# Kernel tuning notes

Measured on AMD Instinct MI355X. Metric: run time of the kernel, lower is better.

Reference implementation:

```python
import jax, jax.numpy as jnp
import numpy as np

SIZE = 1024      # codebook size
DIM = 64         # latent_dim
TOPK = 3
BETA_C = 0.25
LEGACY = False

def setup_inputs() -> dict:
    key = jax.random.key(0)
    kz, ke = jax.random.split(key)
    z = jax.random.normal(kz, (16, 64, 64, DIM), dtype=jnp.float32)
    # nn.Embedding init: uniform(-1/size, 1/size)
    emb = jax.random.uniform(ke, (SIZE, DIM), minval=-1.0 / SIZE, maxval=1.0 / SIZE, dtype=jnp.float32)
    return {"z": z, "emb": emb}

def reference(z, emb):
    zf = z.reshape(-1, DIM)                                  # [N, D]
    # squared euclidean distances via matmul expansion: [N, SIZE]
    d = (jnp.sum(zf ** 2, axis=1, keepdims=True)
         + jnp.sum(emb ** 2, axis=1)
         - 2.0 * (zf @ emb.T))
    neg_d, topk_idx = jax.lax.top_k(-d, TOPK)                # smallest distances -> [N, K]
    # direct gather instead of one-hot matmul (same math)
    z_q = jnp.mean(emb[topk_idx], axis=1).reshape(z.shape)   # [N,K,D] -> [N,D] -> z.shape
    if LEGACY:
        loss = (jnp.mean((jax.lax.stop_gradient(z_q) - z) ** 2)
                + BETA_C * jnp.mean((z_q - jax.lax.stop_gradient(z)) ** 2))
    else:
        loss = (BETA_C * jnp.mean((jax.lax.stop_gradient(z_q) - z) ** 2)
                + jnp.mean((z_q - jax.lax.stop_gradient(z)) ** 2))
    # one-hot encodings are part of the module's return signature
    topk_encodings = jax.nn.one_hot(topk_idx, SIZE, dtype=z.dtype)   # [N, K, SIZE]
    e_mean = jnp.mean(topk_encodings, axis=(0, 1))                   # [SIZE]
    perplexity = jnp.exp(-jnp.sum(e_mean * jnp.log(e_mean + 1e-10)))
    z_q_st = z + jax.lax.stop_gradient(z_q - z)              # straight-through estimator
    return (z_q_st, loss, perplexity, topk_encodings, topk_idx)
```

## Files before the change

kernel.cpp:

```cpp
#include <hip/hip_runtime.h>
#include <math.h>

#define N_ROWS 65536
#define CB 1024
#define SPLITS 4
#define JS (CB / SPLITS)

__device__ __forceinline__ float tree_sum64_sq(const float* x) {
#pragma clang fp contract(off)
    float sq[64];
#pragma unroll
    for (int i = 0; i < 64; ++i) sq[i] = x[i] * x[i];
    float s[16];
#pragma unroll
    for (int l = 0; l < 16; ++l) s[l] = (sq[l] + sq[l + 16]) + (sq[l + 32] + sq[l + 48]);
    float t[8];
#pragma unroll
    for (int l = 0; l < 8; ++l) t[l] = s[l] + s[l + 8];
    float u[4];
#pragma unroll
    for (int l = 0; l < 4; ++l) u[l] = t[l] + t[l + 4];
    float v0 = u[0] + u[2];
    float v1 = u[1] + u[3];
    return v0 + v1;
}

__device__ __forceinline__ void top3_insert(float d, int j,
                                            float& v0, float& v1, float& v2,
                                            int& i0, int& i1, int& i2) {
    bool b0 = d < v0, b1 = d < v1, b2 = d < v2;
    v2 = b1 ? v1 : (b2 ? d : v2);
    i2 = b1 ? i1 : (b2 ? j : i2);
    v1 = b0 ? v0 : (b1 ? d : v1);
    i1 = b0 ? i0 : (b1 ? j : i1);
    v0 = b0 ? d : v0;
    i0 = b0 ? j : i0;
}

__global__ __launch_bounds__(256) void embB_kernel(const float* __restrict__ emb,
                                                   float* __restrict__ B) {
    int j = blockIdx.x * 256 + threadIdx.x;
    if (j >= CB) return;
    float e[64];
    const float4* e4 = (const float4*)(emb + (size_t)j * 64);
#pragma unroll
    for (int k = 0; k < 16; ++k) {
        float4 v = e4[k];
        e[4 * k] = v.x; e[4 * k + 1] = v.y; e[4 * k + 2] = v.z; e[4 * k + 3] = v.w;
    }
    B[j] = tree_sum64_sq(e);
}

__global__ __launch_bounds__(256) void score_kernel(const float* __restrict__ z,
                                                    const float* __restrict__ emb,
                                                    const float* __restrict__ B,
                                                    float* __restrict__ scrD,
                                                    int* __restrict__ scrI) {
    int bid = blockIdx.x;
    int split = bid & (SPLITS - 1);
    int rowBlk = bid >> 2;
    int row = rowBlk * 256 + threadIdx.x;

    float zr[64];
    const float4* z4 = (const float4*)(z + (size_t)row * 64);
#pragma unroll
    for (int k = 0; k < 16; ++k) {
        float4 v = z4[k];
        zr[4 * k] = v.x; zr[4 * k + 1] = v.y; zr[4 * k + 2] = v.z; zr[4 * k + 3] = v.w;
    }
    float A = tree_sum64_sq(zr);

    float v0 = 3.402823466e38f, v1 = 3.402823466e38f, v2 = 3.402823466e38f;
    int i0 = 0, i1 = 0, i2 = 0;
    int jbase = split * JS;

    for (int jj = 0; jj < JS; ++jj) {
        int j = jbase + jj;
        const float4* e4 = (const float4*)(emb + (size_t)j * 64);
        float Bj = B[j];
        float acc = 0.0f;
#pragma unroll
        for (int k = 0; k < 16; ++k) {
            float4 e = e4[k];
            acc = fmaf(zr[4 * k],     e.x, acc);
            acc = fmaf(zr[4 * k + 1], e.y, acc);
            acc = fmaf(zr[4 * k + 2], e.z, acc);
            acc = fmaf(zr[4 * k + 3], e.w, acc);
        }
        float d = (A + Bj) - 2.0f * acc;
        top3_insert(d, j, v0, v1, v2, i0, i1, i2);
    }
    size_t o = ((size_t)split * N_ROWS + row) * 3;
    scrD[o] = v0; scrD[o + 1] = v1; scrD[o + 2] = v2;
    scrI[o] = i0; scrI[o + 1] = i1; scrI[o + 2] = i2;
}

__global__ __launch_bounds__(256) void merge_kernel(const float* __restrict__ z,
                                                    const float* __restrict__ emb,
                                                    const float* __restrict__ scrD,
                                                    const int* __restrict__ scrI,
                                                    float* __restrict__ out0,
                                                    float* __restrict__ out4,
                                                    int* __restrict__ hist,
                                                    float* __restrict__ lossAcc) {
    int row = blockIdx.x * 256 + threadIdx.x;

    float v0 = 3.402823466e38f, v1 = 3.402823466e38f, v2 = 3.402823466e38f;
    int i0 = 0, i1 = 0, i2 = 0;
#pragma unroll
    for (int s = 0; s < SPLITS; ++s) {
        size_t o = ((size_t)s * N_ROWS + row) * 3;
#pragma unroll
        for (int t = 0; t < 3; ++t) {
            float d = scrD[o + t];
            int j = scrI[o + t];
            top3_insert(d, j, v0, v1, v2, i0, i1, i2);
        }
    }

    const float* e0 = emb + (size_t)i0 * 64;
    const float* e1 = emb + (size_t)i1 * 64;
    const float* e2 = emb + (size_t)i2 * 64;
    const float4* z4 = (const float4*)(z + (size_t)row * 64);
    float4* o4 = (float4*)(out0 + (size_t)row * 64);

    float lsum = 0.0f;
#pragma unroll
    for (int k4 = 0; k4 < 16; ++k4) {
        float4 zv = z4[k4];
        float4 st;
        {
            int k = 4 * k4;
            float zq = ((e0[k] + e1[k]) + e2[k]) / 3.0f;
            float df = zq - zv.x;
            st.x = zv.x + df;
            lsum = fmaf(df, df, lsum);
        }
        {
            int k = 4 * k4 + 1;
            float zq = ((e0[k] + e1[k]) + e2[k]) / 3.0f;
            float df = zq - zv.y;
            st.y = zv.y + df;
            lsum = fmaf(df, df, lsum);
        }
        {
            int k = 4 * k4 + 2;
            float zq = ((e0[k] + e1[k]) + e2[k]) / 3.0f;
            float df = zq - zv.z;
            st.z = zv.z + df;
            lsum = fmaf(df, df, lsum);
        }
        {
            int k = 4 * k4 + 3;
            float zq = ((e0[k] + e1[k]) + e2[k]) / 3.0f;
            float df = zq - zv.w;
            st.w = zv.w + df;
            lsum = fmaf(df, df, lsum);
        }
        o4[k4] = st;
    }

    size_t ob = (size_t)row * 3;
    out4[ob]     = (float)i0;
    out4[ob + 1] = (float)i1;
    out4[ob + 2] = (float)i2;
    atomicAdd(&hist[i0], 1);
    atomicAdd(&hist[i1], 1);
    atomicAdd(&hist[i2], 1);

#pragma unroll
    for (int off = 32; off >= 1; off >>= 1) lsum += __shfl_down(lsum, off);
    if ((threadIdx.x & 63) == 0) atomicAdd(lossAcc, lsum);
}

__global__ __launch_bounds__(256) void onehot_kernel(const float* __restrict__ idxf,
                                                     float4* __restrict__ out3) {
    size_t q = (size_t)blockIdx.x * 256 + threadIdx.x;
    int slice = (int)(q >> 8);
    int c0 = (int)(q & 255) * 4;
    int idx = (int)idxf[slice];
    float4 v;
    v.x = (c0     == idx) ? 1.0f : 0.0f;
    v.y = (c0 + 1 == idx) ? 1.0f : 0.0f;
    v.z = (c0 + 2 == idx) ? 1.0f : 0.0f;
    v.w = (c0 + 3 == idx) ? 1.0f : 0.0f;
    out3[q] = v;
}

__global__ __launch_bounds__(256) void finalize_kernel(const int* __restrict__ hist,
                                                       const float* __restrict__ lossAcc,
                                                       float* __restrict__ out1,
                                                       float* __restrict__ out2) {
    __shared__ float red[256];
    int t = threadIdx.x;
    float local = 0.0f;
    for (int b = t; b < CB; b += 256) {
        float em = (float)hist[b] / 196608.0f;
        local += em * logf(em + 1e-10f);
    }
    red[t] = local;
    __syncthreads();
    for (int s = 128; s >= 1; s >>= 1) {
        if (t < s) red[t] += red[t + s];
        __syncthreads();
    }
    if (t == 0) {
        *out2 = expf(-red[0]);
        float m = *lossAcc / 4194304.0f;
        *out1 = 0.25f * m + m;
    }
}

extern "C" void kernel_launch(void* const* d_in, const int* in_sizes, int n_in,
                              void* d_out, int out_size, void* d_ws, size_t ws_size,
                              hipStream_t stream) {
    const float* z   = (const float*)d_in[0];
    const float* emb = (const float*)d_in[1];

    float* out  = (float*)d_out;
    float* out0 = out;
    float* out1 = out + 4194304;
    float* out2 = out + 4194305;
    float* out3 = out + 4194306;
    float* out4 = out + 4194306 + 201326592ll;

    int*   hist    = (int*)d_ws;
    float* lossAcc = (float*)((char*)d_ws + 4096);
    float* B       = (float*)((char*)d_ws + 8192);

    float* scrD = out3;
    int*   scrI = (int*)(out3 + (size_t)SPLITS * N_ROWS * 3);

    hipMemsetAsync(d_ws, 0, 4096 + 16, stream);

    embB_kernel<<<4, 256, 0, stream>>>(emb, B);
    score_kernel<<<(N_ROWS / 256) * SPLITS, 256, 0, stream>>>(z, emb, B, scrD, scrI);
    merge_kernel<<<N_ROWS / 256, 256, 0, stream>>>(z, emb, scrD, scrI, out0, out4,
                                                   hist, lossAcc);
    onehot_kernel<<<196608, 256, 0, stream>>>(out4, (float4*)out3);
    finalize_kernel<<<1, 256, 0, stream>>>(hist, lossAcc, out1, out2);
}
```

Measured before the change: 1.073 ms.

## Fuse score, merge and one-hot kernels into one kernel with interleaved zero-fill

Replaces the split-codebook score kernel, the top-k merge kernel and the one-hot kernel with a single kernel per row block. It scans the full codebook four entries at a time and interleaves zero stores for the block's one-hot region into the distance loop, so the writes overlap the compute. After a barrier it scatters the three ones and reuses the z row held in registers. This drops the scratch round trip, two launches and the separate 800MB one-hot write pass, but cuts grid parallelism fourfold (256 blocks) and relies on the barrier to order zero-fill before the one-hot stores.

```diff
diff --git a/kernel.cpp b/kernel.cpp
--- a/kernel.cpp
+++ b/kernel.cpp
@@ -3,8 +3,6 @@
 
 #define N_ROWS 65536
 #define CB 1024
-#define SPLITS 4
-#define JS (CB / SPLITS)
 
 __device__ __forceinline__ float tree_sum64_sq(const float* x) {
 #pragma clang fp contract(off)
@@ -51,15 +49,16 @@
     B[j] = tree_sum64_sq(e);
 }
 
-__global__ __launch_bounds__(256) void score_kernel(const float* __restrict__ z,
-                                                    const float* __restrict__ emb,
-                                                    const float* __restrict__ B,
-                                                    float* __restrict__ scrD,
-                                                    int* __restrict__ scrI) {
-    int bid = blockIdx.x;
-    int split = bid & (SPLITS - 1);
-    int rowBlk = bid >> 2;
-    int row = rowBlk * 256 + threadIdx.x;
+__global__ __launch_bounds__(256) void mega_kernel(const float* __restrict__ z,
+                                                   const float* __restrict__ emb,
+                                                   const float* __restrict__ B,
+                                                   float* __restrict__ out0,
+                                                   float* __restrict__ out3,
+                                                   float* __restrict__ out4,
+                                                   int* __restrict__ hist,
+                                                   float* __restrict__ lossAcc) {
+    const int t = threadIdx.x;
+    const int row = blockIdx.x * 256 + t;
 
     float zr[64];
     const float4* z4 = (const float4*)(z + (size_t)row * 64);
@@ -70,91 +69,90 @@
     }
     float A = tree_sum64_sq(zr);
 
+    float4* zb = (float4*)out3 + (size_t)blockIdx.x * 196608;
+    const float4 zero4 = make_float4(0.0f, 0.0f, 0.0f, 0.0f);
+
     float v0 = 3.402823466e38f, v1 = 3.402823466e38f, v2 = 3.402823466e38f;
     int i0 = 0, i1 = 0, i2 = 0;
-    int jbase = split * JS;
-
-    for (int jj = 0; jj < JS; ++jj) {
-        int j = jbase + jj;
-        const float4* e4 = (const float4*)(emb + (size_t)j * 64);
-        float Bj = B[j];
-        float acc = 0.0f;
+
+    for (int g = 0; g < 256; ++g) {
+        zb[(size_t)(3 * g + 0) * 256 + t] = zero4;
+        zb[(size_t)(3 * g + 1) * 256 + t] = zero4;
+        zb[(size_t)(3 * g + 2) * 256 + t] = zero4;
+
+        const int j = 4 * g;
+        const float4* e0p = (const float4*)(emb + (size_t)(j + 0) * 64);
+        const float4* e1p = (const float4*)(emb + (size_t)(j + 1) * 64);
+        const float4* e2p = (const float4*)(emb + (size_t)(j + 2) * 64);
+        const float4* e3p = (const float4*)(emb + (size_t)(j + 3) * 64);
+        float b0 = B[j], b1 = B[j + 1], b2 = B[j + 2], b3 = B[j + 3];
+
+        float a0 = 0.0f, a1 = 0.0f, a2 = 0.0f, a3 = 0.0f;
 #pragma unroll
         for (int k = 0; k < 16; ++k) {
-            float4 e = e4[k];
-            acc = fmaf(zr[4 * k],     e.x, acc);
-            acc = fmaf(zr[4 * k + 1], e.y, acc);
-            acc = fmaf(zr[4 * k + 2], e.z, acc);
-            acc = fmaf(zr[4 * k + 3], e.w, acc);
-        }
-        float d = (A + Bj) - 2.0f * acc;
-        top3_insert(d, j, v0, v1, v2, i0, i1, i2);
-    }
-    size_t o = ((size_t)split * N_ROWS + row) * 3;
-    scrD[o] = v0; scrD[o + 1] = v1; scrD[o + 2] = v2;
-    scrI[o] = i0; scrI[o + 1] = i1; scrI[o + 2] = i2;
-}
-
-__global__ __launch_bounds__(256) void merge_kernel(const float* __restrict__ z,
-                                                    const float* __restrict__ emb,
-                                                    const float* __restrict__ scrD,
-                                                    const int* __restrict__ scrI,
-                                                    float* __restrict__ out0,
-                                                    float* __restrict__ out4,
-                                                    int* __restrict__ hist,
-                                                    float* __restrict__ lossAcc) {
-    int row = blockIdx.x * 256 + threadIdx.x;
-
-    float v0 = 3.402823466e38f, v1 = 3.402823466e38f, v2 = 3.402823466e38f;
-    int i0 = 0, i1 = 0, i2 = 0;
-#pragma unroll
-    for (int s = 0; s < SPLITS; ++s) {
-        size_t o = ((size_t)s * N_ROWS + row) * 3;
-#pragma unroll
-        for (int t = 0; t < 3; ++t) {
-            float d = scrD[o + t];
-            int j = scrI[o + t];
-            top3_insert(d, j, v0, v1, v2, i0, i1, i2);
-        }
-    }
+            float4 e0 = e0p[k], e1 = e1p[k], e2 = e2p[k], e3 = e3p[k];
+            float x0 = zr[4 * k], x1 = zr[4 * k + 1], x2 = zr[4 * k + 2], x3 = zr[4 * k + 3];
+            a0 = fmaf(x0, e0.x, a0); a0 = fmaf(x1, e0.y, a0);
+            a0 = fmaf(x2, e0.z, a0); a0 = fmaf(x3, e0.w, a0);
+            a1 = fmaf(x0, e1.x, a1); a1 = fmaf(x1, e1.y, a1);
+            a1 = fmaf(x2, e1.z, a1); a1 = fmaf(x3, e1.w, a1);
+            a2 = fmaf(x0, e2.x, a2); a2 = fmaf(x1, e2.y, a2);
+            a2 = fmaf(x2, e2.z, a2); a2 = fmaf(x3, e2.w, a2);
+            a3 = fmaf(x0, e3.x, a3); a3 = fmaf(x1, e3.y, a3);
+            a3 = fmaf(x2, e3.z, a3); a3 = fmaf(x3, e3.w, a3);
+        }
+        float d0 = (A + b0) - 2.0f * a0;
+        float d1 = (A + b1) - 2.0f * a1;
+        float d2 = (A + b2) - 2.0f * a2;
+        float d3 = (A + b3) - 2.0f * a3;
+        top3_insert(d0, j + 0, v0, v1, v2, i0, i1, i2);
+        top3_insert(d1, j + 1, v0, v1, v2, i0, i1, i2);
+        top3_insert(d2, j + 2, v0, v1, v2, i0, i1, i2);
+        top3_insert(d3, j + 3, v0, v1, v2, i0, i1, i2);
+    }
+
+    __syncthreads();
+
+    size_t rb = (size_t)row * 3072;
+    out3[rb + i0]          = 1.0f;
+    out3[rb + 1024 + i1]   = 1.0f;
+    out3[rb + 2048 + i2]   = 1.0f;
 
     const float* e0 = emb + (size_t)i0 * 64;
     const float* e1 = emb + (size_t)i1 * 64;
     const float* e2 = emb + (size_t)i2 * 64;
-    const float4* z4 = (const float4*)(z + (size_t)row * 64);
     float4* o4 = (float4*)(out0 + (size_t)row * 64);
 
     float lsum = 0.0f;
 #pragma unroll
     for (int k4 = 0; k4 < 16; ++k4) {
-        float4 zv = z4[k4];
         float4 st;
         {
             int k = 4 * k4;
             float zq = ((e0[k] + e1[k]) + e2[k]) / 3.0f;
-            float df = zq - zv.x;
-            st.x = zv.x + df;
+            float df = zq - zr[k];
+            st.x = zr[k] + df;
             lsum = fmaf(df, df, lsum);
         }
         {
             int k = 4 * k4 + 1;
             float zq = ((e0[k] + e1[k]) + e2[k]) / 3.0f;
-            float df = zq - zv.y;
-            st.y = zv.y + df;
+            float df = zq - zr[k];
+            st.y = zr[k] + df;
             lsum = fmaf(df, df, lsum);
         }
         {
             int k = 4 * k4 + 2;
             float zq = ((e0[k] + e1[k]) + e2[k]) / 3.0f;
-            float df = zq - zv.z;
-            st.z = zv.z + df;
+            float df = zq - zr[k];
+            st.z = zr[k] + df;
             lsum = fmaf(df, df, lsum);
         }
         {
             int k = 4 * k4 + 3;
             float zq = ((e0[k] + e1[k]) + e2[k]) / 3.0f;
-            float df = zq - zv.w;
-            st.w = zv.w + df;
+            float df = zq - zr[k];
+            st.w = zr[k] + df;
             lsum = fmaf(df, df, lsum);
         }
         o4[k4] = st;
@@ -170,21 +168,7 @@
 
 #pragma unroll
     for (int off = 32; off >= 1; off >>= 1) lsum += __shfl_down(lsum, off);
-    if ((threadIdx.x & 63) == 0) atomicAdd(lossAcc, lsum);
-}
-
-__global__ __launch_bounds__(256) void onehot_kernel(const float* __restrict__ idxf,
-                                                     float4* __restrict__ out3) {
-    size_t q = (size_t)blockIdx.x * 256 + threadIdx.x;
-    int slice = (int)(q >> 8);
-    int c0 = (int)(q & 255) * 4;
-    int idx = (int)idxf[slice];
-    float4 v;
-    v.x = (c0     == idx) ? 1.0f : 0.0f;
-    v.y = (c0 + 1 == idx) ? 1.0f : 0.0f;
-    v.z = (c0 + 2 == idx) ? 1.0f : 0.0f;
-    v.w = (c0 + 3 == idx) ? 1.0f : 0.0f;
-    out3[q] = v;
+    if ((t & 63) == 0) atomicAdd(lossAcc, lsum);
 }
 
 __global__ __launch_bounds__(256) void finalize_kernel(const int* __restrict__ hist,
@@ -228,15 +212,10 @@
     float* lossAcc = (float*)((char*)d_ws + 4096);
     float* B       = (float*)((char*)d_ws + 8192);
 
-    float* scrD = out3;
-    int*   scrI = (int*)(out3 + (size_t)SPLITS * N_ROWS * 3);
-
     hipMemsetAsync(d_ws, 0, 4096 + 16, stream);
 
     embB_kernel<<<4, 256, 0, stream>>>(emb, B);
-    score_kernel<<<(N_ROWS / 256) * SPLITS, 256, 0, stream>>>(z, emb, B, scrD, scrI);
-    merge_kernel<<<N_ROWS / 256, 256, 0, stream>>>(z, emb, scrD, scrI, out0, out4,
-                                                   hist, lossAcc);
-    onehot_kernel<<<196608, 256, 0, stream>>>(out4, (float4*)out3);
+    mega_kernel<<<N_ROWS / 256, 256, 0, stream>>>(z, emb, B, out0, out3, out4,
+                                                  hist, lossAcc);
     finalize_kernel<<<1, 256, 0, stream>>>(hist, lossAcc, out1, out2);
 }
```

After: 1.712 ms. 1.6x slower.

## Fuse one-hot zero fill into score kernel and scatter ones in merge

Applied to the files above, without the earlier changes.

The separate one-hot kernel that wrote the whole 805MB encodings tensor is removed. The score kernel now interleaves zero-filling its slice of the one-hot output with the distance loop, so those stores overlap with compute, and the merge kernel scatters the three 1.0 entries per row. The scratch top-k buffers move from the output region to the workspace, which avoids a conflict with the zero fill. The inner distance loop is also unrolled over two codebook rows at a time. The change relies on the zero-fill partitioning covering the full tensor and on the workspace being large enough for the scratch buffers.

```diff
diff --git a/kernel.cpp b/kernel.cpp
--- a/kernel.cpp
+++ b/kernel.cpp
@@ -51,15 +51,17 @@
     B[j] = tree_sum64_sq(e);
 }
 
-__global__ __launch_bounds__(256) void score_kernel(const float* __restrict__ z,
-                                                    const float* __restrict__ emb,
-                                                    const float* __restrict__ B,
-                                                    float* __restrict__ scrD,
-                                                    int* __restrict__ scrI) {
-    int bid = blockIdx.x;
-    int split = bid & (SPLITS - 1);
-    int rowBlk = bid >> 2;
-    int row = rowBlk * 256 + threadIdx.x;
+__global__ __launch_bounds__(256) void score_fused_kernel(const float* __restrict__ z,
+                                                          const float* __restrict__ emb,
+                                                          const float* __restrict__ B,
+                                                          float* __restrict__ out3,
+                                                          float* __restrict__ scrD,
+                                                          int* __restrict__ scrI) {
+    const int bid = blockIdx.x;
+    const int split = bid & (SPLITS - 1);
+    const int rowBlk = bid >> 2;
+    const int t = threadIdx.x;
+    const int row = rowBlk * 256 + t;
 
     float zr[64];
     const float4* z4 = (const float4*)(z + (size_t)row * 64);
@@ -70,26 +72,43 @@
     }
     float A = tree_sum64_sq(zr);
 
+    float4* zb = (float4*)out3 + (size_t)rowBlk * 196608 + (size_t)split * 49152;
+    const float4 zero4 = make_float4(0.0f, 0.0f, 0.0f, 0.0f);
+
     float v0 = 3.402823466e38f, v1 = 3.402823466e38f, v2 = 3.402823466e38f;
     int i0 = 0, i1 = 0, i2 = 0;
-    int jbase = split * JS;
-
-    for (int jj = 0; jj < JS; ++jj) {
-        int j = jbase + jj;
-        const float4* e4 = (const float4*)(emb + (size_t)j * 64);
-        float Bj = B[j];
-        float acc = 0.0f;
-#pragma unroll
-        for (int k = 0; k < 16; ++k) {
-            float4 e = e4[k];
-            acc = fmaf(zr[4 * k],     e.x, acc);
-            acc = fmaf(zr[4 * k + 1], e.y, acc);
-            acc = fmaf(zr[4 * k + 2], e.z, acc);
-            acc = fmaf(zr[4 * k + 3], e.w, acc);
-        }
-        float d = (A + Bj) - 2.0f * acc;
-        top3_insert(d, j, v0, v1, v2, i0, i1, i2);
-    }
+    const int jbase = split * JS;
+
+    for (int g = 0; g < 64; ++g) {
+        zb[(size_t)(3 * g + 0) * 256 + t] = zero4;
+        zb[(size_t)(3 * g + 1) * 256 + t] = zero4;
+        zb[(size_t)(3 * g + 2) * 256 + t] = zero4;
+
+#pragma unroll
+        for (int u = 0; u < 4; u += 2) {
+            const int j0 = jbase + 4 * g + u;
+            const int j1 = j0 + 1;
+            const float4* e0p = (const float4*)(emb + (size_t)j0 * 64);
+            const float4* e1p = (const float4*)(emb + (size_t)j1 * 64);
+            float b0v = B[j0], b1v = B[j1];
+            float a0 = 0.0f, a1 = 0.0f;
+#pragma unroll
+            for (int k = 0; k < 16; ++k) {
+                float4 e0 = e0p[k], e1 = e1p[k];
+                float x0 = zr[4 * k], x1 = zr[4 * k + 1];
+                float x2 = zr[4 * k + 2], x3 = zr[4 * k + 3];
+                a0 = fmaf(x0, e0.x, a0); a0 = fmaf(x1, e0.y, a0);
+                a0 = fmaf(x2, e0.z, a0); a0 = fmaf(x3, e0.w, a0);
+                a1 = fmaf(x0, e1.x, a1); a1 = fmaf(x1, e1.y, a1);
+                a1 = fmaf(x2, e1.z, a1); a1 = fmaf(x3, e1.w, a1);
+            }
+            float d0 = (A + b0v) - 2.0f * a0;
+            float d1 = (A + b1v) - 2.0f * a1;
+            top3_insert(d0, j0, v0, v1, v2, i0, i1, i2);
+            top3_insert(d1, j1, v0, v1, v2, i0, i1, i2);
+        }
+    }
+
     size_t o = ((size_t)split * N_ROWS + row) * 3;
     scrD[o] = v0; scrD[o + 1] = v1; scrD[o + 2] = v2;
     scrI[o] = i0; scrI[o + 1] = i1; scrI[o + 2] = i2;
@@ -100,6 +119,7 @@
                                                     const float* __restrict__ scrD,
                                                     const int* __restrict__ scrI,
                                                     float* __restrict__ out0,
+                                                    float* __restrict__ out3,
                                                     float* __restrict__ out4,
                                                     int* __restrict__ hist,
                                                     float* __restrict__ lossAcc) {
@@ -117,6 +137,11 @@
             top3_insert(d, j, v0, v1, v2, i0, i1, i2);
         }
     }
+
+    size_t rb = (size_t)row * 3072;
+    out3[rb + i0]        = 1.0f;
+    out3[rb + 1024 + i1] = 1.0f;
+    out3[rb + 2048 + i2] = 1.0f;
 
     const float* e0 = emb + (size_t)i0 * 64;
     const float* e1 = emb + (size_t)i1 * 64;
@@ -171,20 +196,6 @@
 #pragma unroll
     for (int off = 32; off >= 1; off >>= 1) lsum += __shfl_down(lsum, off);
     if ((threadIdx.x & 63) == 0) atomicAdd(lossAcc, lsum);
-}
-
-__global__ __launch_bounds__(256) void onehot_kernel(const float* __restrict__ idxf,
-                                                     float4* __restrict__ out3) {
-    size_t q = (size_t)blockIdx.x * 256 + threadIdx.x;
-    int slice = (int)(q >> 8);
-    int c0 = (int)(q & 255) * 4;
-    int idx = (int)idxf[slice];
-    float4 v;
-    v.x = (c0     == idx) ? 1.0f : 0.0f;
-    v.y = (c0 + 1 == idx) ? 1.0f : 0.0f;
-    v.z = (c0 + 2 == idx) ? 1.0f : 0.0f;
-    v.w = (c0 + 3 == idx) ? 1.0f : 0.0f;
-    out3[q] = v;
 }
 
 __global__ __launch_bounds__(256) void finalize_kernel(const int* __restrict__ hist,
@@ -227,16 +238,15 @@
     int*   hist    = (int*)d_ws;
     float* lossAcc = (float*)((char*)d_ws + 4096);
     float* B       = (float*)((char*)d_ws + 8192);
-
-    float* scrD = out3;
-    int*   scrI = (int*)(out3 + (size_t)SPLITS * N_ROWS * 3);
+    float* scrD = (float*)((char*)d_ws + 16384);
+    int*   scrI = (int*)((char*)d_ws + 16384 + (size_t)SPLITS * N_ROWS * 3 * 4);
 
     hipMemsetAsync(d_ws, 0, 4096 + 16, stream);
 
     embB_kernel<<<4, 256, 0, stream>>>(emb, B);
-    score_kernel<<<(N_ROWS / 256) * SPLITS, 256, 0, stream>>>(z, emb, B, scrD, scrI);
-    merge_kernel<<<N_ROWS / 256, 256, 0, stream>>>(z, emb, scrD, scrI, out0, out4,
-                                                   hist, lossAcc);
-    onehot_kernel<<<196608, 256, 0, stream>>>(out4, (float4*)out3);
+    score_fused_kernel<<<(N_ROWS / 256) * SPLITS, 256, 0, stream>>>(z, emb, B,
+                                                                    out3, scrD, scrI);
+    merge_kernel<<<N_ROWS / 256, 256, 0, stream>>>(z, emb, scrD, scrI,
+                                                   out0, out3, out4, hist, lossAcc);
     finalize_kernel<<<1, 256, 0, stream>>>(hist, lossAcc, out1, out2);
 }
```

New measurement: 1.182 ms. 1.1x slower.
